# Kernel optimization log

Hardware: AMD Instinct MI355X
Metric: run time of the kernel (lower is better)

Reference implementation:

```python
import jax, jax.numpy as jnp
import numpy as np

TEMPERATURE = 0.07
BASE_TEMPERATURE = 0.07
TOP_K = 15  # epoch=0 branch of the original forward


def _pairwise_dist(a, b):
    # a: [M, D], b: [N, D] -> [M, N] euclidean distance (same math as
    # torch.norm(a.unsqueeze(1) - b.unsqueeze(0), dim=2)), safe at 0.
    sq = (jnp.sum(a * a, axis=-1)[:, None]
          + jnp.sum(b * b, axis=-1)[None, :]
          - 2.0 * (a @ b.T))
    sq = jnp.maximum(sq, 0.0)
    pos = sq > 0.0
    return jnp.where(pos, jnp.sqrt(jnp.where(pos, sq, 1.0)), 0.0)


def setup_inputs() -> dict:
    key = jax.random.key(0)
    k1, k2, k3, k4 = jax.random.split(key, 4)
    B, V, D, N, KMAX = 512, 2, 128, 100000, 50
    features = jax.random.normal(k1, (B, V, D), dtype=jnp.float32)
    saved_features = jax.random.normal(k2, (N, D), dtype=jnp.float32)
    indices = jax.random.randint(k3, (B,), 0, N)
    rks = jax.random.randint(k4, (N, KMAX), 0, N)
    return {"features": features, "indices": indices,
            "saved_features": saved_features, "rks": rks}


def reference(features, indices, saved_features, rks):
    B, V, D = features.shape
    M = V * B
    # torch.cat(torch.unbind(features, dim=1), dim=0)
    contrast = jnp.swapaxes(features, 0, 1).reshape(M, D)
    anchor = contrast  # contrast_mode == 'all'

    d0 = _pairwise_dist(anchor, contrast)                      # [M, M]
    adc_orig = (1.0 + 1.0 / (1.0 + d0)) / TEMPERATURE

    # neighbors_features: mat_k = saved_features[rks[indices, k]], duplicated
    neigh = saved_features[rks[indices, :TOP_K]]               # [B, K, D]
    mats = jnp.swapaxes(neigh, 0, 1)                           # [K, B, D]
    mats = jnp.concatenate([mats, mats], axis=1)               # [K, M, D]

    dk = jax.vmap(lambda m: _pairwise_dist(anchor, m))(mats)   # [K, M, M]
    adck = (1.0 + 1.0 / (1.0 + dk)) / TEMPERATURE

    # p_const = 1 -> plain mean over k; sym accumulation is the transpose
    acc = jnp.sum(adck, axis=0) / TOP_K
    acc_sym = acc.T

    summed = acc ** 2 + acc_sym ** 2 + adc_orig ** 2
    logits_src = jnp.sqrt(summed)  # summed >= adc_orig^2 > 0, sqrt is safe

    logits_max = jax.lax.stop_gradient(jnp.max(logits_src, axis=1, keepdims=True))
    logits = logits_src - logits_max

    mask = jnp.tile(jnp.eye(B, dtype=jnp.float32), (V, V))     # [M, M]
    logits_mask = 1.0 - jnp.eye(M, dtype=jnp.float32)
    mask = mask * logits_mask

    exp_logits = jnp.exp(logits) * logits_mask
    log_prob = logits - jnp.log(jnp.sum(exp_logits, axis=1, keepdims=True))

    mask_pos_pairs = jnp.sum(mask, axis=1)
    mask_pos_pairs = jnp.where(mask_pos_pairs < 1e-6, 1.0, mask_pos_pairs)
    mean_log_prob_pos = jnp.sum(mask * log_prob, axis=1) / mask_pos_pairs

    loss = -(TEMPERATURE / BASE_TEMPERATURE) * mean_log_prob_pos
    return jnp.mean(loss.reshape(V, B))
```

## Files before the change

kernel.cpp:

```cpp
#include <hip/hip_runtime.h>
#include <math.h>

#define BB 512
#define VV 2
#define MM 1024
#define DD 128
#define KMAX 50
#define TOPK 15
#define INV_T (1.0f/0.07f)

#define OFF_ANCH  0
#define OFF_A2    262144
#define OFF_ACCT  266240
#define OFF_PART  (266240 + 2097152)
#define OFF_LSPOS (OFF_PART + 65536)

typedef __attribute__((ext_vector_type(8))) short bf16x8;
typedef __attribute__((ext_vector_type(4))) float f32x4;

__device__ __forceinline__ short f2bf(float x)
{
    union { float f; unsigned u; } a; a.f = x;
    return (short)((a.u + 0x7FFFu + ((a.u >> 16) & 1u)) >> 16);
}

__device__ __forceinline__ bf16x8 cvt8(float4 p0, float4 p1, float& nacc)
{
    float v[8] = {p0.x, p0.y, p0.z, p0.w, p1.x, p1.y, p1.z, p1.w};
    bf16x8 r;
    #pragma unroll
    for (int e = 0; e < 8; ++e) {
        nacc = fmaf(v[e], v[e], nacc);
        r[e] = f2bf(v[e]);
    }
    return r;
}

__global__ __launch_bounds__(256) void k0_anchor(
    const float* __restrict__ feat,
    unsigned* __restrict__ anchor_u,
    float* __restrict__ a2)
{
    const int row  = blockIdx.x * 4 + (threadIdx.x >> 6);
    const int lane = threadIdx.x & 63;
    const int frow = (row & (BB - 1)) * VV + (row >> 9);
    float2 v = *(const float2*)&feat[(size_t)frow * DD + lane * 2];
    unsigned lo = (unsigned)(unsigned short)f2bf(v.x);
    unsigned hi = (unsigned)(unsigned short)f2bf(v.y);
    anchor_u[row * (DD / 2) + lane] = lo | (hi << 16);
    float sq = v.x * v.x + v.y * v.y;
    #pragma unroll
    for (int off = 32; off > 0; off >>= 1) sq += __shfl_xor(sq, off);
    if (lane == 0) a2[row] = sq;
}

__global__ __launch_bounds__(256) void k1_acc(
    const short* __restrict__ anchor,
    const float* __restrict__ a2,
    const int* __restrict__ indices,
    const float* __restrict__ saved, const int* __restrict__ rks,
    float* __restrict__ accT)
{
    const int tid = threadIdx.x;
    const int lane = tid & 63;
    const int wid = tid >> 6;
    const int lr = lane & 15;
    const int lg = lane >> 4;
    const int wr = wid >> 1;
    const int wc = wid & 1;
    const int m0 = blockIdx.x * 64 + wr * 32;

    int aidx[2];
    #pragma unroll
    for (int tm = 0; tm < 2; ++tm) {
        int b = (m0 >> 4) + tm;
        aidx[tm] = rks[(size_t)indices[b] * KMAX + lr];
    }
    bf16x8 af[2][4];
    float nnA[2] = {0.f, 0.f};
    #pragma unroll
    for (int tm = 0; tm < 2; ++tm)
        #pragma unroll
        for (int kc = 0; kc < 4; ++kc) {
            const float4* p = (const float4*)&saved[(size_t)aidx[tm] * DD + kc * 32 + lg * 8];
            af[tm][kc] = cvt8(p[0], p[1], nnA[tm]);
        }
    #pragma unroll
    for (int tm = 0; tm < 2; ++tm) {
        nnA[tm] += __shfl_xor(nnA[tm], 16);
        nnA[tm] += __shfl_xor(nnA[tm], 32);
    }
    float nnAr[2][4];
    #pragma unroll
    for (int tm = 0; tm < 2; ++tm)
        #pragma unroll
        for (int r = 0; r < 4; ++r)
            nnAr[tm][r] = __shfl(nnA[tm], lg * 4 + r);

    #pragma unroll
    for (int jt = 0; jt < 2; ++jt) {
        const int j0 = blockIdx.y * 256 + jt * 128 + wc * 64;
        f32x4 acc[2][4];
        #pragma unroll
        for (int a = 0; a < 2; ++a)
            #pragma unroll
            for (int b = 0; b < 4; ++b) acc[a][b] = (f32x4){0.f, 0.f, 0.f, 0.f};
        #pragma unroll
        for (int kc = 0; kc < 4; ++kc) {
            bf16x8 bf[4];
            #pragma unroll
            for (int tn = 0; tn < 4; ++tn)
                bf[tn] = *(const bf16x8*)&anchor[(size_t)(j0 + tn * 16 + lr) * DD + kc * 32 + lg * 8];
            #pragma unroll
            for (int tm = 0; tm < 2; ++tm)
                #pragma unroll
                for (int tn = 0; tn < 4; ++tn)
                    acc[tm][tn] = __builtin_amdgcn_mfma_f32_16x16x32_bf16(
                        af[tm][kc], bf[tn], acc[tm][tn], 0, 0, 0);
        }
        #pragma unroll
        for (int tm = 0; tm < 2; ++tm) {
            const int b = (m0 >> 4) + tm;
            #pragma unroll
            for (int tn = 0; tn < 4; ++tn) {
                const float a2j = a2[j0 + tn * 16 + lr];
                float s = 0.f;
                #pragma unroll
                for (int r = 0; r < 4; ++r) {
                    float g = acc[tm][tn][r];
                    float sq = fmaxf(fmaf(-2.f, g, a2j + nnAr[tm][r]), 0.f);
                    float d = __builtin_amdgcn_sqrtf(sq);
                    float f = fmaf(__builtin_amdgcn_rcpf(1.f + d), INV_T, INV_T);
                    if (lg == 3 && r == 3) f = 0.f;
                    s += f;
                }
                s += __shfl_xor(s, 16);
                s += __shfl_xor(s, 32);
                if (lane < 16)
                    accT[(size_t)b * MM + j0 + tn * 16 + lane] = s * (1.0f / TOPK);
            }
        }
    }
}

__global__ __launch_bounds__(256) void k2_exp(
    const short* __restrict__ anchor, const float* __restrict__ a2,
    const float* __restrict__ accT,
    float* __restrict__ part, float* __restrict__ lspos)
{
    __shared__ float pshare[4][16];
    const int tid = threadIdx.x;
    const int lane = tid & 63;
    const int wid = tid >> 6;
    const int lr = lane & 15;
    const int lg = lane >> 4;
    const int i0 = blockIdx.x * 16;
    const int jg = blockIdx.y;
    const int jcol = jg * 64 + wid * 16 + lr;

    f32x4 acc = (f32x4){0.f, 0.f, 0.f, 0.f};
    #pragma unroll
    for (int kc = 0; kc < 4; ++kc) {
        bf16x8 af = *(const bf16x8*)&anchor[(size_t)(i0 + lr) * DD + kc * 32 + lg * 8];
        bf16x8 bf = *(const bf16x8*)&anchor[(size_t)jcol * DD + kc * 32 + lg * 8];
        acc = __builtin_amdgcn_mfma_f32_16x16x32_bf16(af, bf, acc, 0, 0, 0);
    }
    const int ib4 = i0 + lg * 4;
    const float4 a2i4 = *(const float4*)&a2[ib4];
    const float a2iv[4] = {a2i4.x, a2i4.y, a2i4.z, a2i4.w};
    const float a2j = a2[jcol];
    const float4 aij4 = *(const float4*)&accT[(size_t)(jcol & (BB - 1)) * MM + ib4];
    const float aijv[4] = {aij4.x, aij4.y, aij4.z, aij4.w};

    float esum[4];
    #pragma unroll
    for (int r = 0; r < 4; ++r) {
        const int i = ib4 + r;
        float g = acc[r];
        float sq = fmaxf(fmaf(-2.f, g, a2iv[r] + a2j), 0.f);
        float d0 = __builtin_amdgcn_sqrtf(sq);
        float adc = fmaf(__builtin_amdgcn_rcpf(1.f + d0), INV_T, INV_T);
        float aji = accT[(size_t)(i & (BB - 1)) * MM + jcol];
        float ls = __builtin_amdgcn_sqrtf(aijv[r] * aijv[r] + aji * aji + adc * adc);
        esum[r] = (jcol == i) ? 0.f : __expf(ls);
        if (jcol == (i ^ BB)) lspos[i] = ls;
    }
    #pragma unroll
    for (int r = 0; r < 4; ++r) {
        float e = esum[r];
        e += __shfl_xor(e, 1);
        e += __shfl_xor(e, 2);
        e += __shfl_xor(e, 4);
        e += __shfl_xor(e, 8);
        if (lr == 0) pshare[wid][lg * 4 + r] = e;
    }
    __syncthreads();
    if (tid < 16)
        part[(size_t)(i0 + tid) * 16 + jg] =
            pshare[0][tid] + pshare[1][tid] + pshare[2][tid] + pshare[3][tid];
}

__global__ __launch_bounds__(256) void k3_finish(
    const float* __restrict__ part, const float* __restrict__ lspos,
    float* __restrict__ out)
{
    __shared__ float red[4];
    const int tid = threadIdx.x;
    const int lane = tid & 63, w = tid >> 6;
    float lsum = 0.f;
    #pragma unroll
    for (int q = 0; q < 4; ++q) {
        const int i = tid + q * 256;
        float s = 0.f;
        #pragma unroll
        for (int jg = 0; jg < 16; ++jg) s += part[(size_t)i * 16 + jg];
        lsum += __logf(s) - lspos[i];
    }
    #pragma unroll
    for (int off = 32; off > 0; off >>= 1) lsum += __shfl_xor(lsum, off);
    if (lane == 0) red[w] = lsum;
    __syncthreads();
    if (tid == 0) out[0] = (red[0] + red[1] + red[2] + red[3]) * (1.0f / MM);
}

extern "C" void kernel_launch(void* const* d_in, const int* in_sizes, int n_in,
                              void* d_out, int out_size, void* d_ws, size_t ws_size,
                              hipStream_t stream)
{
    const float* feat    = (const float*)d_in[0];
    const int*   indices = (const int*)  d_in[1];
    const float* saved   = (const float*)d_in[2];
    const int*   rks     = (const int*)  d_in[3];

    char* w = (char*)d_ws;
    short* anchor = (short*)(w + OFF_ANCH);
    float* a2     = (float*)(w + OFF_A2);
    float* accT   = (float*)(w + OFF_ACCT);
    float* part   = (float*)(w + OFF_PART);
    float* lspos  = (float*)(w + OFF_LSPOS);

    k0_anchor<<<MM / 4, 256, 0, stream>>>(feat, (unsigned*)anchor, a2);
    k1_acc<<<dim3(128, 4), 256, 0, stream>>>(anchor, a2, indices, saved, rks, accT);
    k2_exp<<<dim3(64, 16), 256, 0, stream>>>(anchor, a2, accT, part, lspos);
    k3_finish<<<1, 256, 0, stream>>>(part, lspos, (float*)d_out);
}
```

Before: 35.39 us.

## Prefetch gathered neighbor rows in k0 and stage them through LDS in k1

k0 now also issues dummy loads of the gathered saved_features rows so they are warm in L2 (or MALL) before k1 runs. k1 loads each neighbor row once per block cooperatively with coalesced float4 reads, converts it to bf16 in padded LDS, and computes norms there. Previously each wave gathered its rows with scattered per-lane loads. This cuts k1's latency on random gathers, at the cost of extra prefetch traffic in k0 and an LDS barrier in k1.

Measured after the change: 34.28 us, median of 2. 3.2% less time.

```diff
diff --git a/kernel.cpp b/kernel.cpp
--- a/kernel.cpp
+++ b/kernel.cpp
@@ -18,31 +18,36 @@
 typedef __attribute__((ext_vector_type(8))) short bf16x8;
 typedef __attribute__((ext_vector_type(4))) float f32x4;
 
+#define PADS 132
+
 __device__ __forceinline__ short f2bf(float x)
 {
     union { float f; unsigned u; } a; a.f = x;
     return (short)((a.u + 0x7FFFu + ((a.u >> 16) & 1u)) >> 16);
 }
 
-__device__ __forceinline__ bf16x8 cvt8(float4 p0, float4 p1, float& nacc)
-{
-    float v[8] = {p0.x, p0.y, p0.z, p0.w, p1.x, p1.y, p1.z, p1.w};
-    bf16x8 r;
-    #pragma unroll
-    for (int e = 0; e < 8; ++e) {
-        nacc = fmaf(v[e], v[e], nacc);
-        r[e] = f2bf(v[e]);
-    }
-    return r;
-}
-
 __global__ __launch_bounds__(256) void k0_anchor(
     const float* __restrict__ feat,
+    const int* __restrict__ indices,
+    const int* __restrict__ rks,
+    const float* __restrict__ saved,
     unsigned* __restrict__ anchor_u,
     float* __restrict__ a2)
 {
-    const int row  = blockIdx.x * 4 + (threadIdx.x >> 6);
-    const int lane = threadIdx.x & 63;
+    const int tid = threadIdx.x;
+
+    {
+        const int pr = blockIdx.x * 256 + tid;
+        const int b = pr & 511;
+        int k = (pr >> 9) & 15; if (k > 14) k = 14;
+        const int c = pr >> 13;
+        const int idx = rks[(size_t)indices[b] * KMAX + k];
+        float4 t4 = *(const float4*)&saved[(size_t)idx * DD + c * 16];
+        asm volatile("" :: "v"(t4.x), "v"(t4.y), "v"(t4.z), "v"(t4.w));
+    }
+
+    const int row  = blockIdx.x * 4 + (tid >> 6);
+    const int lane = tid & 63;
     const int frow = (row & (BB - 1)) * VV + (row >> 9);
     float2 v = *(const float2*)&feat[(size_t)frow * DD + lane * 2];
     unsigned lo = (unsigned)(unsigned short)f2bf(v.x);
@@ -61,41 +66,58 @@
     const float* __restrict__ saved, const int* __restrict__ rks,
     float* __restrict__ accT)
 {
-    const int tid = threadIdx.x;
+    __shared__ short As[64 * PADS];
+    __shared__ float nrm[64];
+
+    const int tid = threadIdx.x;
+
+    {
+        const int row = tid >> 2;
+        const int seg = tid & 3;
+        const int grow = blockIdx.x * 64 + row;
+        const int b = grow >> 4;
+        int k = grow & 15; if (k > 14) k = 14;
+        const int idx = rks[(size_t)indices[b] * KMAX + k];
+        const float4* src = (const float4*)&saved[(size_t)idx * DD + seg * 32];
+        unsigned* dst = (unsigned*)&As[row * PADS + seg * 32];
+        float pn = 0.f;
+        #pragma unroll
+        for (int c = 0; c < 8; ++c) {
+            float4 v = src[c];
+            pn = fmaf(v.x, v.x, fmaf(v.y, v.y, fmaf(v.z, v.z, fmaf(v.w, v.w, pn))));
+            unsigned p0 = (unsigned)(unsigned short)f2bf(v.x)
+                        | ((unsigned)(unsigned short)f2bf(v.y) << 16);
+            unsigned p1 = (unsigned)(unsigned short)f2bf(v.z)
+                        | ((unsigned)(unsigned short)f2bf(v.w) << 16);
+            dst[c * 2 + 0] = p0;
+            dst[c * 2 + 1] = p1;
+        }
+        pn += __shfl_xor(pn, 1);
+        pn += __shfl_xor(pn, 2);
+        if (seg == 0) nrm[row] = pn;
+    }
+    __syncthreads();
+
     const int lane = tid & 63;
     const int wid = tid >> 6;
     const int lr = lane & 15;
     const int lg = lane >> 4;
     const int wr = wid >> 1;
     const int wc = wid & 1;
-    const int m0 = blockIdx.x * 64 + wr * 32;
-
-    int aidx[2];
-    #pragma unroll
-    for (int tm = 0; tm < 2; ++tm) {
-        int b = (m0 >> 4) + tm;
-        aidx[tm] = rks[(size_t)indices[b] * KMAX + lr];
-    }
+    const int lrow0 = wr * 32;
+
     bf16x8 af[2][4];
-    float nnA[2] = {0.f, 0.f};
     #pragma unroll
     for (int tm = 0; tm < 2; ++tm)
         #pragma unroll
-        for (int kc = 0; kc < 4; ++kc) {
-            const float4* p = (const float4*)&saved[(size_t)aidx[tm] * DD + kc * 32 + lg * 8];
-            af[tm][kc] = cvt8(p[0], p[1], nnA[tm]);
-        }
-    #pragma unroll
-    for (int tm = 0; tm < 2; ++tm) {
-        nnA[tm] += __shfl_xor(nnA[tm], 16);
-        nnA[tm] += __shfl_xor(nnA[tm], 32);
-    }
+        for (int kc = 0; kc < 4; ++kc)
+            af[tm][kc] = *(const bf16x8*)&As[(lrow0 + tm * 16 + lr) * PADS + kc * 32 + lg * 8];
     float nnAr[2][4];
     #pragma unroll
     for (int tm = 0; tm < 2; ++tm)
         #pragma unroll
         for (int r = 0; r < 4; ++r)
-            nnAr[tm][r] = __shfl(nnA[tm], lg * 4 + r);
+            nnAr[tm][r] = nrm[lrow0 + tm * 16 + lg * 4 + r];
 
     #pragma unroll
     for (int jt = 0; jt < 2; ++jt) {
@@ -118,6 +140,7 @@
                     acc[tm][tn] = __builtin_amdgcn_mfma_f32_16x16x32_bf16(
                         af[tm][kc], bf[tn], acc[tm][tn], 0, 0, 0);
         }
+        const int m0 = blockIdx.x * 64 + lrow0;
         #pragma unroll
         for (int tm = 0; tm < 2; ++tm) {
             const int b = (m0 >> 4) + tm;
@@ -239,7 +262,8 @@
     float* part   = (float*)(w + OFF_PART);
     float* lspos  = (float*)(w + OFF_LSPOS);
 
-    k0_anchor<<<MM / 4, 256, 0, stream>>>(feat, (unsigned*)anchor, a2);
+    k0_anchor<<<MM / 4, 256, 0, stream>>>(feat, indices, rks, saved,
+                                          (unsigned*)anchor, a2);
     k1_acc<<<dim3(128, 4), 256, 0, stream>>>(anchor, a2, indices, saved, rks, accT);
     k2_exp<<<dim3(64, 16), 256, 0, stream>>>(anchor, a2, accT, part, lspos);
     k3_finish<<<1, 256, 0, stream>>>(part, lspos, (float*)d_out);
```
